# Kernel optimization log

Measured on AMD Instinct MI355X. Metric: run time of the kernel, lower is better.

## Reference

```python
import jax, jax.numpy as jnp
import numpy as np


def _expand_chunk(x):
    # prepend the previous bucket along the chunk axis: [b, nb, bl, ...] -> [b, nb, 2*bl, ...]
    return jnp.concatenate([jnp.roll(x, 1, axis=1), x], axis=2)


def _gather_seq(origin, idx):
    # origin [b, s, d], idx [b, s, r] -> out[b, s, :, r] = origin[b, idx[b, s, r], :]
    b = origin.shape[0]
    g = origin[jnp.arange(b)[:, None, None], idx]  # [b, s, r, d]
    return jnp.transpose(g, (0, 1, 3, 2))          # [b, s, d, r]


def _count_dup_keys(inp, rounds):
    # inp [b, s, K] int32: count duplicate key indices within a window of `rounds` in sorted order
    sort_idx = jnp.argsort(inp, axis=2)
    sorted_k = jnp.take_along_axis(inp, sort_idx, axis=2)
    unsort = jnp.argsort(sort_idx, axis=2)
    cnt = jnp.ones(inp.shape, jnp.float32)
    for i in range(1, rounds):
        eq = (sorted_k[..., i:] == sorted_k[..., :-i]).astype(jnp.float32)
        pad = jnp.zeros(inp.shape[:-1] + (i,), jnp.float32)
        cnt = cnt + jnp.concatenate([pad, eq], axis=-1) + jnp.concatenate([eq, pad], axis=-1)
    return jnp.take_along_axis(cnt, unsort, axis=2)


def setup_inputs() -> dict:
    key = jax.random.key(0)
    k1, k2, k3 = jax.random.split(key, 3)
    B_M_H, SEQ, D_K, N_ROUNDS, N_BUCKETS = 32, 2048, 64, 4, 32
    query = jax.random.normal(k1, (B_M_H, SEQ, D_K), jnp.float32)
    value = jax.random.normal(k2, (B_M_H, SEQ, D_K), jnp.float32)
    rand_matrix = jax.random.normal(k3, (B_M_H, D_K, N_ROUNDS, N_BUCKETS // 2), jnp.float32)
    return {"query": query, "value": value, "rand_matrix": rand_matrix}


def reference(query, value, rand_matrix):
    b, s, d = query.shape
    nr = rand_matrix.shape[2]
    n_buckets = 2 * rand_matrix.shape[3]
    bl = s // n_buckets  # bucket_len

    # --- LSH hashing: argmax over [proj, -proj], then make hashes unique per position ---
    proj = jnp.einsum('bsd,bdrk->bsrk', query, rand_matrix)
    hashes = jnp.argmax(jnp.concatenate([proj, -proj], axis=-1), axis=-1).astype(jnp.int32)
    hashes = hashes * s + jnp.arange(s, dtype=jnp.int32)[None, :, None]  # [b, s, nr]

    sort_idx = jnp.argsort(hashes, axis=1)      # [b, s, nr]
    unsort_idx = jnp.argsort(sort_idx, axis=1)  # [b, s, nr]

    # --- sort queries into buckets ---
    q = _gather_seq(query, sort_idx).reshape(b, n_buckets, bl, d, nr)
    k = _expand_chunk(q)  # [b, nb, 2*bl, d, nr]
    k = k * jax.lax.rsqrt(jnp.maximum(jnp.sum(k * k, axis=-2, keepdims=True), 1e-12))

    qk = jnp.einsum('bnidr,bnjdr->bnijr', q, k) / np.float32(np.sqrt(d))  # [b, nb, bl, 2bl, nr]

    # --- causal / self masks on original positions ---
    qi = sort_idx.reshape(b, n_buckets, bl, nr) % s
    ki = _expand_chunk(qi)  # [b, nb, 2bl, nr]
    mask1 = (qi[:, :, :, None, :] < ki[:, :, None, :, :]).astype(jnp.float32)
    mask2 = (qi[:, :, :, None, :] == ki[:, :, None, :, :]).astype(jnp.float32)
    qk = qk * (1 - mask1) + mask1 * (-1e9)
    qk = qk * (1 - mask2) + mask2 * (-1e5)

    # --- duplicate-key counting across rounds ---
    ki_b = jnp.broadcast_to(ki[:, :, None, :, :], (b, n_buckets, bl, 2 * bl, nr)).reshape(b, s, 2 * bl * nr)
    count_keys = _count_dup_keys(ki_b, nr).reshape(b, s, 2 * bl, nr)

    qk = qk.reshape(b, s, 2 * bl, nr)
    lse = jax.scipy.special.logsumexp(qk, axis=2)  # [b, s, nr]
    sm = jnp.exp(qk - lse[:, :, None, :]) / count_keys

    v = _gather_seq(value, sort_idx).reshape(b, n_buckets, bl, d, nr)
    vk = _expand_chunk(v)  # [b, nb, 2bl, d, nr]
    sm = sm.reshape(b, n_buckets, bl, 2 * bl, nr)
    att = jnp.einsum('bnijr,bnjdr->bnidr', sm, vk).reshape(b, s, d, nr)

    # --- unsort back to original order, per round ---
    att = jnp.transpose(att, (0, 1, 3, 2))  # [b, s, nr, d]
    att = jnp.take_along_axis(att, jnp.broadcast_to(unsort_idx[:, :, :, None], att.shape), axis=1)
    lse = jnp.take_along_axis(lse, unsort_idx, axis=1)

    # --- combine rounds weighted by softmax of logsumexp ---
    w = jax.nn.softmax(lse, axis=-1)  # [b, s, nr]
    return jnp.einsum('bsrd,bsr->bsd', att, w)
```

## Files before the change

### kernel.cpp

```cpp
#include <hip/hip_runtime.h>

typedef unsigned short u16;
typedef unsigned int   u32;
typedef short bf16x8 __attribute__((ext_vector_type(8)));
typedef float f32x16 __attribute__((ext_vector_type(16)));

#define S_  2048
#define D_  64
#define NR_ 4
#define NB_ 32

#define AS 72
#define VS 136
#define PS 136

__device__ __forceinline__ float bf2f(u16 u){ return __uint_as_float(((u32)u)<<16); }
__device__ __forceinline__ u16 f2bf(float f){
  u32 u = __float_as_uint(f);
  u32 r = (u + 0x7fffu + ((u>>16)&1u)) >> 16;
  return (u16)r;
}
__device__ __forceinline__ u32 pk2bf(float a, float b){
#if __has_builtin(__builtin_amdgcn_cvt_pk_bf16_f32)
  auto r = __builtin_amdgcn_cvt_pk_bf16_f32(a, b);
  u32 u; __builtin_memcpy(&u, &r, 4); return u;
#else
  return (u32)f2bf(a) | ((u32)f2bf(b) << 16);
#endif
}
__device__ __forceinline__ u16 f2bf1(float a){ return (u16)pk2bf(a, a); }
__device__ __forceinline__ void unpack2(u32 w, float &a, float &b){
  a = __uint_as_float(w<<16);
  b = __uint_as_float(w & 0xffff0000u);
}
__device__ __forceinline__ bf16x8 ld8(const u16* p){
  union { uint4 u; bf16x8 v; } x;
  x.u = *(const uint4*)p;
  return x.v;
}

__global__ __launch_bounds__(256, 2) void k_hash(const float* __restrict__ q,
                                                 const float* __restrict__ v,
                                                 const float* __restrict__ R,
                                                 int* __restrict__ hout,
                                                 u16* __restrict__ qb,
                                                 u16* __restrict__ vbuf,
                                                 float* __restrict__ scq){
  __shared__ float Rl[4096];
  int b   = blockIdx.x >> 3;
  int pos = (blockIdx.x & 7) * 256 + threadIdx.x;

  {
    const float4* Rg = (const float4*)(R + (size_t)b * 4096);
    float4* Rs = (float4*)Rl;
    #pragma unroll
    for (int k = 0; k < 4; k++) Rs[k*256 + threadIdx.x] = Rg[k*256 + threadIdx.x];
  }
  __syncthreads();

  const float4* q4 = (const float4*)(q + ((size_t)b * S_ + pos) * D_);
  const float4* v4 = (const float4*)(v + ((size_t)b * S_ + pos) * D_);
  uint2* qw = (uint2*)(qb   + ((size_t)b * S_ + pos) * D_);
  uint2* vw = (uint2*)(vbuf + ((size_t)b * S_ + pos) * D_);

  float acc[64];
  #pragma unroll
  for (int i = 0; i < 64; i++) acc[i] = 0.f;
  float ss = 0.f;

  #pragma unroll 4
  for (int c = 0; c < 16; c++){
    float4 wa = q4[c];
    float4 xa = v4[c];
    ss += wa.x*wa.x + wa.y*wa.y + wa.z*wa.z + wa.w*wa.w;
    qw[c] = make_uint2(pk2bf(wa.x, wa.y), pk2bf(wa.z, wa.w));
    vw[c] = make_uint2(pk2bf(xa.x, xa.y), pk2bf(xa.z, xa.w));
    float qa[4] = {wa.x, wa.y, wa.z, wa.w};
    #pragma unroll
    for (int dd = 0; dd < 4; dd++){
      int d = c * 4 + dd;
      const float4* Rr = (const float4*)(&Rl[d * 64]);
      #pragma unroll
      for (int k4 = 0; k4 < 16; k4++){
        float4 rv = Rr[k4];
        acc[k4*4+0] += qa[dd] * rv.x;
        acc[k4*4+1] += qa[dd] * rv.y;
        acc[k4*4+2] += qa[dd] * rv.z;
        acc[k4*4+3] += qa[dd] * rv.w;
      }
    }
  }
  scq[(size_t)b * S_ + pos] = rsqrtf(fmaxf(ss, 1e-12f)) * 0.125f;

  #pragma unroll
  for (int r = 0; r < 4; r++){
    float bv = acc[r*16]; int bi = 0;
    #pragma unroll
    for (int m = 1; m < 32; m++){
      float vv = (m < 16) ? acc[r*16 + m] : -acc[r*16 + m - 16];
      if (vv > bv){ bv = vv; bi = m; }
    }
    hout[((size_t)b * NR_ + r) * S_ + pos] = bi;
  }
}

__global__ __launch_bounds__(256) void k_sort(const int* __restrict__ h,
                                              int* __restrict__ sidx,
                                              int* __restrict__ chk){
  __shared__ int cnt[32][257];
  __shared__ int base[32];
  int br = blockIdx.x;
  const int* hb = h + (size_t)br * S_;
  int t = threadIdx.x;

  #pragma unroll
  for (int hh = 0; hh < 32; hh++) cnt[hh][t] = 0;
  __syncthreads();

  int hv[8];
  const int4* hb4 = (const int4*)hb;
  int4 a0 = hb4[t*2], a1 = hb4[t*2+1];
  hv[0]=a0.x; hv[1]=a0.y; hv[2]=a0.z; hv[3]=a0.w;
  hv[4]=a1.x; hv[5]=a1.y; hv[6]=a1.z; hv[7]=a1.w;
  #pragma unroll
  for (int k = 0; k < 8; k++) cnt[hv[k]][t]++;
  __syncthreads();

  int wave = t >> 6, lane = t & 63;
  for (int hh = wave*8; hh < wave*8 + 8; hh++){
    int vals[4]; int s0 = 0;
    #pragma unroll
    for (int k = 0; k < 4; k++){ vals[k] = cnt[hh][lane*4+k]; s0 += vals[k]; }
    int incl = s0;
    #pragma unroll
    for (int off = 1; off < 64; off <<= 1){
      int o = __shfl_up(incl, off, 64);
      if (lane >= off) incl += o;
    }
    int run = incl - s0;
    #pragma unroll
    for (int k = 0; k < 4; k++){ int tmp = vals[k]; cnt[hh][lane*4+k] = run; run += tmp; }
    if (lane == 63) base[hh] = incl;
  }
  __syncthreads();
  if (t == 0){
    int run = 0;
    #pragma unroll
    for (int hh = 0; hh < 32; hh++){ int tot = base[hh]; base[hh] = run; run += tot; }
  }
  __syncthreads();

  int p0 = t * 8;
  #pragma unroll
  for (int k = 0; k < 8; k++){
    int hh = hv[k];
    int c = cnt[hh][t];
    int slot = base[hh] + c;
    cnt[hh][t] = c + 1;
    sidx[(size_t)br * S_ + slot]    = p0 + k;
    chk [(size_t)br * S_ + p0 + k]  = slot >> 6;
  }
}

__global__ __launch_bounds__(256, 3) void k_attn(const u16* __restrict__ qb,
                                                 const u16* __restrict__ vb,
                                                 const int* __restrict__ sidx,
                                                 const int* __restrict__ chk,
                                                 const float* __restrict__ scq,
                                                 float* __restrict__ lse_ws,
                                                 u16*  __restrict__ att_ws){
  __shared__ u16 A[128*AS];
  __shared__ u16 SM[64*PS];
  __shared__ int   pkey[128];
  __shared__ float rcnt[128];
  __shared__ float sc[128];
  __shared__ float pm[4*64];
  __shared__ float ps[4*64];

  int blk = blockIdx.x;
  int b = blk >> 7, r = (blk >> 5) & 3, n = blk & 31;
  int npv = (n + 31) & 31;
  int t = threadIdx.x;
  int lane = t & 63, w = t >> 6;
  int la = lane & 31, hh = lane >> 5;
  int coff = hh * 8;
  const int* sb = sidx + ((size_t)b * NR_ + r) * S_;

  if (t < 128){
    int p = (t < 64) ? sb[npv*64 + t] : sb[n*64 + (t - 64)];
    pkey[t] = p;
    int c = 0;
    #pragma unroll
    for (int rr = 0; rr < 4; rr++){
      int ch = chk[((size_t)b * NR_ + rr) * S_ + p];
      c += (ch == n) || (ch == npv);
    }
    if (c < 1) c = 1;
    rcnt[t] = 1.0f / (float)c;
    sc[t] = scq[(size_t)b * S_ + p];
  }
  __syncthreads();

  {
    int row = t >> 1, half = t & 1;
    const uint4* src = (const uint4*)(qb + ((size_t)b*S_ + pkey[row])*D_) + half*4;
    uint4* dst = (uint4*)(&A[row*AS + half*32]);
    #pragma unroll
    for (int k = 0; k < 4; k++) dst[k] = src[k];
  }
  int jp = t & 63, dgrp = t >> 6;
  uint4 va0, va1, vb0, vb1;
  {
    const uint4* s0 = (const uint4*)(vb + ((size_t)b*S_ + pkey[2*jp  ])*D_ + dgrp*16);
    const uint4* s1 = (const uint4*)(vb + ((size_t)b*S_ + pkey[2*jp+1])*D_ + dgrp*16);
    va0 = s0[0]; va1 = s0[1]; vb0 = s1[0]; vb1 = s1[1];
  }
  __syncthreads();

  float e0[16], e1[16];
  float ml0, ml1;
  {
    int jt = w;
    f32x16 acc0, acc1;
    #pragma unroll
    for (int i = 0; i < 16; i++){ acc0[i] = 0.f; acc1[i] = 0.f; }
    int arow  = (jt*32 + la) * AS;
    int brow0 = (64 + la) * AS;
    int brow1 = (96 + la) * AS;
    #pragma unroll
    for (int ks = 0; ks < 4; ks++){
      int o = ks*16 + coff;
      bf16x8 af = ld8(&A[arow  + o]);
      bf16x8 b0 = ld8(&A[brow0 + o]);
      bf16x8 b1 = ld8(&A[brow1 + o]);
      acc0 = __builtin_amdgcn_mfma_f32_32x32x16_bf16(af, b0, acc0, 0, 0, 0);
      acc1 = __builtin_amdgcn_mfma_f32_32x32x16_bf16(af, b1, acc1, 0, 0, 0);
    }
    int pj[16]; float scj[16];
    #pragma unroll
    for (int g = 0; g < 4; g++){
      int j0 = jt*32 + g*8 + 4*hh;
      #pragma unroll
      for (int m = 0; m < 4; m++){ pj[g*4+m] = pkey[j0+m]; scj[g*4+m] = sc[j0+m]; }
    }
    int pi0 = pkey[64 + la], pi1 = pkey[96 + la];
    float x0[16], x1[16];
    #pragma unroll
    for (int reg = 0; reg < 16; reg++){
      float a0v = acc0[reg] * scj[reg];
      float a1v = acc1[reg] * scj[reg];
      if (pi0 < pj[reg]) a0v = -1000000000.0f; else if (pi0 == pj[reg]) a0v = -100000.0f;
      if (pi1 < pj[reg]) a1v = -1000000000.0f; else if (pi1 == pj[reg]) a1v = -100000.0f;
      x0[reg] = a0v; x1[reg] = a1v;
    }
    ml0 = x0[0]; ml1 = x1[0];
    #pragma unroll
    for (int reg = 1; reg < 16; reg++){ ml0 = fmaxf(ml0, x0[reg]); ml1 = fmaxf(ml1, x1[reg]); }
    float s0 = 0.f, s1 = 0.f;
    #pragma unroll
    for (int reg = 0; reg < 16; reg++){
      e0[reg] = __expf(x0[reg] - ml0); s0 += e0[reg];
      e1[reg] = __expf(x1[reg] - ml1); s1 += e1[reg];
    }
    float om0 = __shfl_xor(ml0, 32, 64), os0 = __shfl_xor(s0, 32, 64);
    float om1 = __shfl_xor(ml1, 32, 64), os1 = __shfl_xor(s1, 32, 64);
    float m20 = fmaxf(ml0, om0);
    float m21 = fmaxf(ml1, om1);
    float s20 = s0 * __expf(ml0 - m20) + os0 * __expf(om0 - m20);
    float s21 = s1 * __expf(ml1 - m21) + os1 * __expf(om1 - m21);
    if (hh == 0){
      pm[jt*64 + la]      = m20;  ps[jt*64 + la]      = s20;
      pm[jt*64 + 32 + la] = m21;  ps[jt*64 + 32 + la] = s21;
    }
  }
  __syncthreads();

  {
    int jt = w;
    float mg0 = pm[la],      mg1 = pm[32 + la];
    #pragma unroll
    for (int k = 1; k < 4; k++){
      mg0 = fmaxf(mg0, pm[k*64 + la]);
      mg1 = fmaxf(mg1, pm[k*64 + 32 + la]);
    }
    float sg0 = 0.f, sg1 = 0.f;
    #pragma unroll
    for (int k = 0; k < 4; k++){
      sg0 += ps[k*64 + la]      * __expf(pm[k*64 + la]      - mg0);
      sg1 += ps[k*64 + 32 + la] * __expf(pm[k*64 + 32 + la] - mg1);
    }
    float f0 = __expf(ml0 - mg0) / sg0;
    float f1 = __expf(ml1 - mg1) / sg1;
    #pragma unroll
    for (int g = 0; g < 4; g++){
      int j0 = jt*32 + g*8 + 4*hh;
      float4 rc = *(const float4*)(&rcnt[j0]);
      float p00 = e0[g*4+0]*f0*rc.x, p01 = e0[g*4+1]*f0*rc.y;
      float p02 = e0[g*4+2]*f0*rc.z, p03 = e0[g*4+3]*f0*rc.w;
      float p10 = e1[g*4+0]*f1*rc.x, p11 = e1[g*4+1]*f1*rc.y;
      float p12 = e1[g*4+2]*f1*rc.z, p13 = e1[g*4+3]*f1*rc.w;
      *(uint2*)(&SM[la*PS + j0])        = make_uint2(pk2bf(p00,p01), pk2bf(p02,p03));
      *(uint2*)(&SM[(32+la)*PS + j0])   = make_uint2(pk2bf(p10,p11), pk2bf(p12,p13));
    }
    if (w == 0 && hh == 0){
      lse_ws[((size_t)b*S_ + pkey[64 + la])*NR_ + r] = mg0 + __logf(sg0);
      lse_ws[((size_t)b*S_ + pkey[96 + la])*NR_ + r] = mg1 + __logf(sg1);
    }
  }
  {
    u32 au[8] = {va0.x, va0.y, va0.z, va0.w, va1.x, va1.y, va1.z, va1.w};
    u32 bu[8] = {vb0.x, vb0.y, vb0.z, vb0.w, vb1.x, vb1.y, vb1.z, vb1.w};
    u32* vtp = (u32*)A;
    #pragma unroll
    for (int k = 0; k < 8; k++){
      int d0 = dgrp*16 + 2*k;
      u32 even = (au[k] & 0xffffu) | (bu[k] << 16);
      u32 odd  = (au[k] >> 16)     | (bu[k] & 0xffff0000u);
      vtp[ d0      * (VS/2) + jp] = even;
      vtp[(d0 + 1) * (VS/2) + jp] = odd;
    }
  }
  __syncthreads();

  {
    int Mt2 = w >> 1, Nt2 = w & 1;
    f32x16 acc;
    #pragma unroll
    for (int i = 0; i < 16; i++) acc[i] = 0.f;
    int arow = (Mt2*32 + la) * VS;
    int brow = (Nt2*32 + la) * PS;
    #pragma unroll
    for (int ks = 0; ks < 8; ks++){
      int o = ks*16 + coff;
      bf16x8 af = ld8(&A[arow + o]);
      bf16x8 bf = ld8(&SM[brow + o]);
      acc = __builtin_amdgcn_mfma_f32_32x32x16_bf16(af, bf, acc, 0, 0, 0);
    }
    int i = Nt2*32 + la;
    int p = pkey[64 + i];
    u16* base = att_ws + (((size_t)b*S_ + p)*NR_ + r)*D_ + Mt2*32 + 4*hh;
    #pragma unroll
    for (int g = 0; g < 4; g++){
      uint2 val = make_uint2(pk2bf(acc[4*g+0], acc[4*g+1]),
                             pk2bf(acc[4*g+2], acc[4*g+3]));
      *(uint2*)(base + g*8) = val;
    }
  }
}

__global__ __launch_bounds__(256) void k_comb(const float* __restrict__ lse_ws,
                                              const u16* __restrict__ att_ws,
                                              float* __restrict__ out){
  size_t idx4 = (size_t)blockIdx.x * 256 + threadIdx.x;
  size_t pd = idx4 >> 4;
  int d0 = (int)(idx4 & 15) * 4;
  float4 lv = *(const float4*)(lse_ws + pd * 4);
  float m = fmaxf(fmaxf(lv.x, lv.y), fmaxf(lv.z, lv.w));
  float e0 = __expf(lv.x - m), e1 = __expf(lv.y - m);
  float e2 = __expf(lv.z - m), e3 = __expf(lv.w - m);
  float inv = 1.0f / (e0 + e1 + e2 + e3);
  e0 *= inv; e1 *= inv; e2 *= inv; e3 *= inv;
  const u16* a = att_ws + pd * 256 + d0;
  uint2 u0 = *(const uint2*)(a);
  uint2 u1 = *(const uint2*)(a + 64);
  uint2 u2 = *(const uint2*)(a + 128);
  uint2 u3 = *(const uint2*)(a + 192);
  float4 o;
  float a0,b0,a1,b1,a2,b2,a3,b3;
  unpack2(u0.x,a0,b0); unpack2(u1.x,a1,b1); unpack2(u2.x,a2,b2); unpack2(u3.x,a3,b3);
  o.x = a0*e0 + a1*e1 + a2*e2 + a3*e3;
  o.y = b0*e0 + b1*e1 + b2*e2 + b3*e3;
  unpack2(u0.y,a0,b0); unpack2(u1.y,a1,b1); unpack2(u2.y,a2,b2); unpack2(u3.y,a3,b3);
  o.z = a0*e0 + a1*e1 + a2*e2 + a3*e3;
  o.w = b0*e0 + b1*e1 + b2*e2 + b3*e3;
  *(float4*)(out + pd * D_ + d0) = o;
}

extern "C" void kernel_launch(void* const* d_in, const int* in_sizes, int n_in,
                              void* d_out, int out_size, void* d_ws, size_t ws_size,
                              hipStream_t stream){
  const float* q = (const float*)d_in[0];
  const float* v = (const float*)d_in[1];
  const float* R = (const float*)d_in[2];

  char* w = (char*)d_ws;
  int*   h    = (int*)  (w + 0);
  int*   sidx = (int*)  (w + (size_t)(1u << 20));
  int*   chkA = (int*)  (w + (size_t)(2u << 20));
  float* lse  = (float*)(w + (size_t)(3u << 20));
  u16*   att  = (u16*)  (w + (size_t)(4u << 20));
  u16*   qb   = (u16*)  (w + (size_t)(36u << 20));
  u16*   vbuf = (u16*)  (w + (size_t)(44u << 20));
  float* scq  = (float*)(w + (size_t)(52u << 20));
  float* out  = (float*)d_out;

  k_hash <<<256,  256, 0, stream>>>(q, v, R, h, qb, vbuf, scq);
  k_sort <<<128,  256, 0, stream>>>(h, sidx, chkA);
  k_attn <<<4096, 256, 0, stream>>>(qb, vbuf, sidx, chkA, scq, lse, att);
  k_comb <<<4096, 256, 0, stream>>>(lse, att, out);
}
```

Measured before the change: 149.0 us.

## Split hash projection rounds across wavefronts with four positions per thread

Reorganizes k_hash so each wavefront handles one hashing round (16 projection columns) for four sequence positions per lane, instead of each thread computing all 64 columns for one position. Wave 0 handles the query bf16 conversion and norm, and wave 1 handles the value conversion. This divides the LDS reads of the random matrix by four per position and lets the same query loads feed four rounds' worth of work across waves. The cost is that every wave reloads the query rows and the bf16 stores are serialized onto only two waves.

```diff
diff --git a/kernel.cpp b/kernel.cpp
--- a/kernel.cpp
+++ b/kernel.cpp
@@ -47,60 +47,95 @@
                                                  u16* __restrict__ vbuf,
                                                  float* __restrict__ scq){
   __shared__ float Rl[4096];
-  int b   = blockIdx.x >> 3;
-  int pos = (blockIdx.x & 7) * 256 + threadIdx.x;
+  int b    = blockIdx.x >> 3;
+  int pbas = (blockIdx.x & 7) * 256;
+  int t    = threadIdx.x;
+  int w    = t >> 6;
+  int lane = t & 63;
 
   {
     const float4* Rg = (const float4*)(R + (size_t)b * 4096);
     float4* Rs = (float4*)Rl;
     #pragma unroll
-    for (int k = 0; k < 4; k++) Rs[k*256 + threadIdx.x] = Rg[k*256 + threadIdx.x];
-  }
-  __syncthreads();
-
-  const float4* q4 = (const float4*)(q + ((size_t)b * S_ + pos) * D_);
-  const float4* v4 = (const float4*)(v + ((size_t)b * S_ + pos) * D_);
-  uint2* qw = (uint2*)(qb   + ((size_t)b * S_ + pos) * D_);
-  uint2* vw = (uint2*)(vbuf + ((size_t)b * S_ + pos) * D_);
-
-  float acc[64];
-  #pragma unroll
-  for (int i = 0; i < 64; i++) acc[i] = 0.f;
-  float ss = 0.f;
-
-  #pragma unroll 4
+    for (int k = 0; k < 4; k++) Rs[k*256 + t] = Rg[k*256 + t];
+  }
+  __syncthreads();
+
+  const float4* q4[4];
+  const float4* v4[4];
+  uint2* qw[4];
+  uint2* vw[4];
+  int pos[4];
+  #pragma unroll
+  for (int i = 0; i < 4; i++){
+    pos[i] = pbas + i*64 + lane;
+    size_t off = ((size_t)b * S_ + pos[i]) * D_;
+    q4[i] = (const float4*)(q + off);
+    v4[i] = (const float4*)(v + off);
+    qw[i] = (uint2*)(qb   + off);
+    vw[i] = (uint2*)(vbuf + off);
+  }
+
+  float acc[4][16];
+  #pragma unroll
+  for (int i = 0; i < 4; i++)
+    #pragma unroll
+    for (int k = 0; k < 16; k++) acc[i][k] = 0.f;
+  float ss[4] = {0.f, 0.f, 0.f, 0.f};
+
+  #pragma unroll 2
   for (int c = 0; c < 16; c++){
-    float4 wa = q4[c];
-    float4 xa = v4[c];
-    ss += wa.x*wa.x + wa.y*wa.y + wa.z*wa.z + wa.w*wa.w;
-    qw[c] = make_uint2(pk2bf(wa.x, wa.y), pk2bf(wa.z, wa.w));
-    vw[c] = make_uint2(pk2bf(xa.x, xa.y), pk2bf(xa.z, xa.w));
-    float qa[4] = {wa.x, wa.y, wa.z, wa.w};
+    float4 qv[4];
+    #pragma unroll
+    for (int i = 0; i < 4; i++) qv[i] = q4[i][c];
+    if (w == 0){
+      #pragma unroll
+      for (int i = 0; i < 4; i++){
+        float4 f = qv[i];
+        ss[i] += f.x*f.x + f.y*f.y + f.z*f.z + f.w*f.w;
+        qw[i][c] = make_uint2(pk2bf(f.x, f.y), pk2bf(f.z, f.w));
+      }
+    } else if (w == 1){
+      #pragma unroll
+      for (int i = 0; i < 4; i++){
+        float4 x = v4[i][c];
+        vw[i][c] = make_uint2(pk2bf(x.x, x.y), pk2bf(x.z, x.w));
+      }
+    }
     #pragma unroll
     for (int dd = 0; dd < 4; dd++){
       int d = c * 4 + dd;
-      const float4* Rr = (const float4*)(&Rl[d * 64]);
+      const float4* Rr = (const float4*)(&Rl[d * 64 + w * 16]);
       #pragma unroll
-      for (int k4 = 0; k4 < 16; k4++){
+      for (int k4 = 0; k4 < 4; k4++){
         float4 rv = Rr[k4];
-        acc[k4*4+0] += qa[dd] * rv.x;
-        acc[k4*4+1] += qa[dd] * rv.y;
-        acc[k4*4+2] += qa[dd] * rv.z;
-        acc[k4*4+3] += qa[dd] * rv.w;
+        #pragma unroll
+        for (int i = 0; i < 4; i++){
+          float qa = (dd == 0) ? qv[i].x : (dd == 1) ? qv[i].y
+                   : (dd == 2) ? qv[i].z : qv[i].w;
+          acc[i][k4*4+0] += qa * rv.x;
+          acc[i][k4*4+1] += qa * rv.y;
+          acc[i][k4*4+2] += qa * rv.z;
+          acc[i][k4*4+3] += qa * rv.w;
+        }
       }
     }
   }
-  scq[(size_t)b * S_ + pos] = rsqrtf(fmaxf(ss, 1e-12f)) * 0.125f;
-
-  #pragma unroll
-  for (int r = 0; r < 4; r++){
-    float bv = acc[r*16]; int bi = 0;
+  if (w == 0){
+    #pragma unroll
+    for (int i = 0; i < 4; i++)
+      scq[(size_t)b * S_ + pos[i]] = rsqrtf(fmaxf(ss[i], 1e-12f)) * 0.125f;
+  }
+
+  #pragma unroll
+  for (int i = 0; i < 4; i++){
+    float bv = acc[i][0]; int bi = 0;
     #pragma unroll
     for (int m = 1; m < 32; m++){
-      float vv = (m < 16) ? acc[r*16 + m] : -acc[r*16 + m - 16];
+      float vv = (m < 16) ? acc[i][m] : -acc[i][m - 16];
       if (vv > bv){ bv = vv; bi = m; }
     }
-    hout[((size_t)b * NR_ + r) * S_ + pos] = bi;
+    hout[((size_t)b * NR_ + w) * S_ + pos[i]] = bi;
   }
 }
 
```

New measurement: 180.8 us. 21.3% more time.
